# Kernel tuning notes

Measured on AMD Instinct MI355X. Metric: run time of the kernel, lower is better.

The kernel has to match this reference:

```python
import jax, jax.numpy as jnp
import numpy as np

N = 500000     # total nodes across all sets
DIM = 128      # input feature dim
HID = 128      # hidden_dim (output of key_net/val_net)
KDIM = 128     # key_storage.encoder.input_dim
MID = 128      # build_mlp mid width (midmult=1.0 -> (in+out)/2)
NB = 4096      # n_batches

def mish(x):
    return x * jnp.tanh(jax.nn.softplus(x))

def layernorm(x, g, b):
    mu = jnp.mean(x, axis=-1, keepdims=True)
    var = jnp.var(x, axis=-1, keepdims=True)
    return (x - mu) * jax.lax.rsqrt(var + 1e-5) * g + b

def mlp2(x, W1, b1, g, bn, W2, b2):
    # build_mlp(nlayers=2, layernorm=True, nonlinearity=Mish)
    h = layernorm(x @ W1 + b1, g, bn)
    return mish(h) @ W2 + b2

def seg_softmax(x, batch, n):
    # scatter_softmax over the node axis within each segment, per feature
    m = jax.ops.segment_max(x, batch, num_segments=n)
    e = jnp.exp(x - m[batch])
    d = jax.ops.segment_sum(e, batch, num_segments=n)
    return e / d[batch]

def _init(key, fan_in, shape):
    return jax.random.normal(key, shape, dtype=jnp.float32) / np.sqrt(fan_in)

def setup_inputs():
    key = jax.random.key(0)
    ks = jax.random.split(key, 12)
    return {
        "x": jax.random.normal(ks[0], (N, DIM), dtype=jnp.float32),
        "batch": jnp.sort(jax.random.randint(ks[1], (N,), 0, NB)),
        "n_batches": NB,
        # mapping: Linear(dim -> KDIM)
        "W_map": _init(ks[2], DIM, (DIM, KDIM)), "b_map": jnp.zeros(KDIM, jnp.float32),
        # key_net: KDIM -> MID -> HID
        "kW1": _init(ks[3], KDIM, (KDIM, MID)), "kb1": jnp.zeros(MID, jnp.float32),
        "kg": jnp.ones(MID, jnp.float32), "kbn": jnp.zeros(MID, jnp.float32),
        "kW2": _init(ks[4], MID, (MID, HID)), "kb2": jnp.zeros(HID, jnp.float32),
        # val_net: DIM -> MID -> HID
        "vW1": _init(ks[5], DIM, (DIM, MID)), "vb1": jnp.zeros(MID, jnp.float32),
        "vg": jnp.ones(MID, jnp.float32), "vbn": jnp.zeros(MID, jnp.float32),
        "vW2": _init(ks[6], MID, (MID, HID)), "vb2": jnp.zeros(HID, jnp.float32),
        # inner key_storage encoder params (same structure, on keys)
        "iW_map": _init(ks[7], KDIM, (KDIM, KDIM)), "ib_map": jnp.zeros(KDIM, jnp.float32),
        "ikW1": _init(ks[8], KDIM, (KDIM, MID)), "ikb1": jnp.zeros(MID, jnp.float32),
        "ikg": jnp.ones(MID, jnp.float32), "ikbn": jnp.zeros(MID, jnp.float32),
        "ikW2": _init(ks[9], MID, (MID, HID)), "ikb2": jnp.zeros(HID, jnp.float32),
        "ivW1": _init(ks[10], KDIM, (KDIM, MID)), "ivb1": jnp.zeros(MID, jnp.float32),
        "ivg": jnp.ones(MID, jnp.float32), "ivbn": jnp.zeros(MID, jnp.float32),
        "ivW2": _init(ks[11], MID, (MID, HID)), "ivb2": jnp.zeros(HID, jnp.float32),
    }

def reference(x, batch, n_batches, W_map, b_map, kW1, kb1, kg, kbn, kW2, kb2,
              vW1, vb1, vg, vbn, vW2, vb2, iW_map, ib_map,
              ikW1, ikb1, ikg, ikbn, ikW2, ikb2, ivW1, ivb1, ivg, ivbn, ivW2, ivb2):
    # key0 = mapping(x); keys = scatter_softmax(key0, batch)
    key0 = x @ W_map + b_map                      # [N, KDIM]
    keys = seg_softmax(key0, batch, n_batches)    # [N, KDIM]
    # y = val_net(x) * key_net(keys); z = scatter_sum(y, batch)
    y = mlp2(x, vW1, vb1, vg, vbn, vW2, vb2) * mlp2(keys, kW1, kb1, kg, kbn, kW2, kb2)
    z = jax.ops.segment_sum(y, batch, num_segments=n_batches)   # [NB, HID]
    # keyenc = key_storage.encoder(keys, batch): same encoder math applied to keys
    key0b = keys @ iW_map + ib_map
    keys2 = seg_softmax(key0b, batch, n_batches)
    y2 = mlp2(keys, ivW1, ivb1, ivg, ivbn, ivW2, ivb2) * mlp2(keys2, ikW1, ikb1, ikg, ikbn, ikW2, ikb2)
    keyenc = jax.ops.segment_sum(y2, batch, num_segments=n_batches)  # [NB, HID]
    return (z, keyenc)
```

## Files before the change

### kernel.cpp

```cpp
#include <hip/hip_runtime.h>

typedef _Float16 f16;
typedef _Float16 f16x4 __attribute__((ext_vector_type(4)));
typedef _Float16 f16x8 __attribute__((ext_vector_type(8)));
typedef float f32x4 __attribute__((ext_vector_type(4)));

#define NBATCH 4096
#define RMAX 200

__device__ __forceinline__ f32x4 mfma16(f16x8 a, f16x8 b, f32x4 c) {
  return __builtin_amdgcn_mfma_f32_16x16x32_f16(a, b, c, 0, 0, 0);
}

__device__ __forceinline__ int swz(int r, int c) { return r * 128 + (c ^ ((r & 7) << 3)); }

__global__ void seg_bounds(const int* __restrict__ batch, int N, int NB, int* __restrict__ seg) {
  int s = blockIdx.x * blockDim.x + threadIdx.x;
  if (s > NB) return;
  int lo = 0, hi = N;
  while (lo < hi) { int mid = (lo + hi) >> 1; if (batch[mid] < s) lo = mid + 1; else hi = mid; }
  seg[s] = lo;
}

__global__ void pack_weights(const float* w0, const float* w1, const float* w2, const float* w3,
                             const float* w4, const float* w5, const float* w6, const float* w7,
                             const float* w8, const float* w9, f16* __restrict__ Wp) {
  int idx = blockIdx.x * blockDim.x + threadIdx.x;
  if (idx >= 10 * 16384) return;
  int w = idx >> 14, p = idx & 16383;
  int j = p & 7, lane = (p >> 3) & 63, nt = (p >> 9) & 7, kk = p >> 12;
  int k = kk * 32 + (lane >> 4) * 8 + j;
  int n = nt * 16 + (lane & 15);
  const float* W;
  switch (w) {
    case 0: W = w0; break; case 1: W = w1; break; case 2: W = w2; break;
    case 3: W = w3; break; case 4: W = w4; break; case 5: W = w5; break;
    case 6: W = w6; break; case 7: W = w7; break; case 8: W = w8; break;
    default: W = w9; break;
  }
  Wp[idx] = (f16)W[k * 128 + n];
}

__device__ __forceinline__ void gemm_bias_phase(const f16* S, f16* D, const f16* __restrict__ Wg,
    const float* __restrict__ bias, int rows, int mq, int nq, int lane, int quad, int li) {
  int ntl = (rows + 15) >> 4;
  const f16* wb0 = Wg + (size_t)(((nq * 2 + 0) * 64 + lane) * 8);
  const f16* wb1 = Wg + (size_t)(((nq * 2 + 1) * 64 + lane) * 8);
  float bc0 = bias[(nq * 2 + 0) * 16 + li];
  float bc1 = bias[(nq * 2 + 1) * 16 + li];
  for (int t = mq; t < ntl; t += 4) {
    int m0 = t * 16;
    f32x4 acc0 = {0.f, 0.f, 0.f, 0.f}, acc1 = {0.f, 0.f, 0.f, 0.f};
    int rl = m0 + li;
    bool ok = rl < rows;
#pragma unroll
    for (int kk = 0; kk < 4; ++kk) {
      f16x8 aF = {};
      if (ok) aF = *(const f16x8*)(S + swz(rl, kk * 32 + quad * 8));
      f16x8 b0 = *(const f16x8*)(wb0 + kk * 4096);
      f16x8 b1 = *(const f16x8*)(wb1 + kk * 4096);
      acc0 = mfma16(aF, b0, acc0);
      acc1 = mfma16(aF, b1, acc1);
    }
#pragma unroll
    for (int r = 0; r < 4; ++r) {
      int row = m0 + quad * 4 + r;
      if (row < rows) {
        D[swz(row, (nq * 2) * 16 + li)] = (f16)(acc0[r] + bc0);
        D[swz(row, (nq * 2 + 1) * 16 + li)] = (f16)(acc1[r] + bc1);
      }
    }
  }
}

__device__ __forceinline__ void ln_mish_pass(f16* D, const float* __restrict__ g,
                                             const float* __restrict__ bn, int rows, int tid) {
  int part = tid & 7;
  int cbase = part * 16;
  for (int r = tid >> 3; r < rows; r += 128) {
    f16x8 v0 = *(const f16x8*)(D + swz(r, cbase));
    f16x8 v1 = *(const f16x8*)(D + swz(r, cbase + 8));
    float f[16];
#pragma unroll
    for (int e = 0; e < 8; ++e) { f[e] = (float)v0[e]; f[8 + e] = (float)v1[e]; }
    float s1 = 0.f, s2 = 0.f;
#pragma unroll
    for (int e = 0; e < 16; ++e) { s1 += f[e]; s2 = fmaf(f[e], f[e], s2); }
    s1 += __shfl_xor(s1, 1, 64); s2 += __shfl_xor(s2, 1, 64);
    s1 += __shfl_xor(s1, 2, 64); s2 += __shfl_xor(s2, 2, 64);
    s1 += __shfl_xor(s1, 4, 64); s2 += __shfl_xor(s2, 4, 64);
    float mean = s1 * (1.f / 128.f);
    float var = s2 * (1.f / 128.f) - mean * mean;
    float rstd = rsqrtf(var + 1e-5f);
    float mr = -mean * rstd;
    f16x8 o0, o1;
#pragma unroll
    for (int e = 0; e < 16; ++e) {
      float gv = g[cbase + e];
      float bv = bn[cbase + e];
      float u = fmaf(fmaf(f[e], rstd, mr), gv, bv);
      float t = __expf(u);
      float w = t * t + 2.f * t;
      float res = (u > 20.f) ? u : u * (w / (w + 2.f));
      if (e < 8) o0[e] = (f16)res; else o1[e - 8] = (f16)res;
    }
    *(f16x8*)(D + swz(r, cbase)) = o0;
    *(f16x8*)(D + swz(r, cbase + 8)) = o1;
  }
}

__device__ __forceinline__ void softmax_phase(f16* P, int rows, int tid,
                                              float* __restrict__ pm, float* __restrict__ mbuf) {
  int cg = tid & 15, st = tid >> 4;
  int c8 = cg * 8;
  int wv = tid >> 6;
  f16x8 NEGV;
#pragma unroll
  for (int e = 0; e < 8; ++e) NEGV[e] = (f16)(-65504.f);
  int r0 = st, r1 = st + 64, r2 = st + 128, r3 = st + 192;
  f16x8 v0 = (r0 < rows) ? *(const f16x8*)(P + swz(r0, c8)) : NEGV;
  f16x8 v1 = (r1 < rows) ? *(const f16x8*)(P + swz(r1, c8)) : NEGV;
  f16x8 v2 = (r2 < rows) ? *(const f16x8*)(P + swz(r2, c8)) : NEGV;
  f16x8 v3 = (r3 < rows) ? *(const f16x8*)(P + swz(r3, c8)) : NEGV;
  float m8[8];
#pragma unroll
  for (int e = 0; e < 8; ++e) {
    float a = (float)v0[e], b = (float)v1[e], c = (float)v2[e], d = (float)v3[e];
    m8[e] = fmaxf(fmaxf(a, b), fmaxf(c, d));
    m8[e] = fmaxf(m8[e], __shfl_xor(m8[e], 16, 64));
    m8[e] = fmaxf(m8[e], __shfl_xor(m8[e], 32, 64));
  }
  if ((tid & 63) < 16) {
    float4 pa = {m8[0], m8[1], m8[2], m8[3]}, pb = {m8[4], m8[5], m8[6], m8[7]};
    *(float4*)(pm + wv * 128 + c8) = pa;
    *(float4*)(pm + wv * 128 + c8 + 4) = pb;
  }
  __syncthreads();
  if (tid < 128) {
    float M = pm[tid];
#pragma unroll
    for (int w = 1; w < 16; ++w) M = fmaxf(M, pm[w * 128 + tid]);
    mbuf[tid] = M;
  }
  __syncthreads();
  float M8[8];
  {
    float4 a = *(const float4*)(mbuf + c8);
    float4 b = *(const float4*)(mbuf + c8 + 4);
    M8[0] = a.x; M8[1] = a.y; M8[2] = a.z; M8[3] = a.w;
    M8[4] = b.x; M8[5] = b.y; M8[6] = b.z; M8[7] = b.w;
  }
  float d8[8];
#pragma unroll
  for (int e = 0; e < 8; ++e) {
    float s = __expf((float)v0[e] - M8[e]) + __expf((float)v1[e] - M8[e]) +
              __expf((float)v2[e] - M8[e]) + __expf((float)v3[e] - M8[e]);
    s += __shfl_xor(s, 16, 64);
    s += __shfl_xor(s, 32, 64);
    d8[e] = s;
  }
  __syncthreads();
  if ((tid & 63) < 16) {
    float4 pa = {d8[0], d8[1], d8[2], d8[3]}, pb = {d8[4], d8[5], d8[6], d8[7]};
    *(float4*)(pm + wv * 128 + c8) = pa;
    *(float4*)(pm + wv * 128 + c8 + 4) = pb;
  }
  __syncthreads();
  if (tid < 128) {
    float Dv = 0.f;
#pragma unroll
    for (int w = 0; w < 16; ++w) Dv += pm[w * 128 + tid];
    mbuf[tid] = (Dv > 0.f) ? 1.f / Dv : 0.f;
  }
  __syncthreads();
  float I8[8];
  {
    float4 a = *(const float4*)(mbuf + c8);
    float4 b = *(const float4*)(mbuf + c8 + 4);
    I8[0] = a.x; I8[1] = a.y; I8[2] = a.z; I8[3] = a.w;
    I8[4] = b.x; I8[5] = b.y; I8[6] = b.z; I8[7] = b.w;
  }
  if (r0 < rows) {
    f16x8 o;
#pragma unroll
    for (int e = 0; e < 8; ++e) o[e] = (f16)(__expf((float)v0[e] - M8[e]) * I8[e]);
    *(f16x8*)(P + swz(r0, c8)) = o;
  }
  if (r1 < rows) {
    f16x8 o;
#pragma unroll
    for (int e = 0; e < 8; ++e) o[e] = (f16)(__expf((float)v1[e] - M8[e]) * I8[e]);
    *(f16x8*)(P + swz(r1, c8)) = o;
  }
  if (r2 < rows) {
    f16x8 o;
#pragma unroll
    for (int e = 0; e < 8; ++e) o[e] = (f16)(__expf((float)v2[e] - M8[e]) * I8[e]);
    *(f16x8*)(P + swz(r2, c8)) = o;
  }
  if (r3 < rows) {
    f16x8 o;
#pragma unroll
    for (int e = 0; e < 8; ++e) o[e] = (f16)(__expf((float)v3[e] - M8[e]) * I8[e]);
    *(f16x8*)(P + swz(r3, c8)) = o;
  }
}

__device__ __forceinline__ void pairsum_phase(const f16* S1, const f16* __restrict__ W1,
    const float* __restrict__ b1, const f16* S2, const f16* __restrict__ W2,
    const float* __restrict__ b2, float* __restrict__ outp, int s, int rows,
    int mq, int nq, int lane, int quad, int li, float* red, int tid) {
  const f16* w10 = W1 + (size_t)(((nq * 2 + 0) * 64 + lane) * 8);
  const f16* w11 = W1 + (size_t)(((nq * 2 + 1) * 64 + lane) * 8);
  const f16* w20 = W2 + (size_t)(((nq * 2 + 0) * 64 + lane) * 8);
  const f16* w21 = W2 + (size_t)(((nq * 2 + 1) * 64 + lane) * 8);
  float b1c0 = b1[(nq * 2 + 0) * 16 + li], b1c1 = b1[(nq * 2 + 1) * 16 + li];
  float b2c0 = b2[(nq * 2 + 0) * 16 + li], b2c1 = b2[(nq * 2 + 1) * 16 + li];
  float zs0 = 0.f, zs1 = 0.f;
  int ntl = (rows + 15) >> 4;
  for (int t = mq; t < ntl; t += 4) {
    int m0 = t * 16;
    f32x4 a10 = {0.f,0.f,0.f,0.f}, a11 = {0.f,0.f,0.f,0.f};
    f32x4 a20 = {0.f,0.f,0.f,0.f}, a21 = {0.f,0.f,0.f,0.f};
    int rl = m0 + li;
    bool ok = rl < rows;
#pragma unroll
    for (int kk = 0; kk < 4; ++kk) {
      f16x8 aF1 = {}, aF2 = {};
      if (ok) {
        aF1 = *(const f16x8*)(S1 + swz(rl, kk * 32 + quad * 8));
        aF2 = *(const f16x8*)(S2 + swz(rl, kk * 32 + quad * 8));
      }
      a10 = mfma16(aF1, *(const f16x8*)(w10 + kk * 4096), a10);
      a11 = mfma16(aF1, *(const f16x8*)(w11 + kk * 4096), a11);
      a20 = mfma16(aF2, *(const f16x8*)(w20 + kk * 4096), a20);
      a21 = mfma16(aF2, *(const f16x8*)(w21 + kk * 4096), a21);
    }
    float cs0 = 0.f, cs1 = 0.f;
#pragma unroll
    for (int r = 0; r < 4; ++r) {
      int row = m0 + quad * 4 + r;
      if (row < rows) {
        cs0 += (a10[r] + b1c0) * (a20[r] + b2c0);
        cs1 += (a11[r] + b1c1) * (a21[r] + b2c1);
      }
    }
    cs0 += __shfl_xor(cs0, 16, 64); cs0 += __shfl_xor(cs0, 32, 64);
    cs1 += __shfl_xor(cs1, 16, 64); cs1 += __shfl_xor(cs1, 32, 64);
    zs0 += cs0; zs1 += cs1;
  }
  if (quad == 0) {
    red[mq * 128 + nq * 32 + li] = zs0;
    red[mq * 128 + nq * 32 + 16 + li] = zs1;
  }
  __syncthreads();
  if (tid < 128) {
    float ssum = red[tid] + red[128 + tid] + red[256 + tid] + red[384 + tid];
    outp[(size_t)s * 128 + tid] = ssum;
  }
  __syncthreads();
}

__global__ __launch_bounds__(1024)
__attribute__((amdgpu_waves_per_eu(4, 4)))
void encoder_mega(
    const float* __restrict__ x, const int* __restrict__ seg, const f16* __restrict__ Wp,
    const float* b_map, const float* kb1, const float* kg, const float* kbn, const float* kb2,
    const float* vb1, const float* vg, const float* vbn, const float* vb2,
    const float* ib_map, const float* ikb1, const float* ikg, const float* ikbn,
    const float* ikb2, const float* ivb1, const float* ivg, const float* ivbn,
    const float* ivb2, float* __restrict__ Z, float* __restrict__ KE) {
  __shared__ f16 L0[RMAX * 128];
  __shared__ f16 L1[RMAX * 128];
  __shared__ f16 L2[RMAX * 128];
  __shared__ float pm[16 * 128];
  __shared__ float mbuf[128];
  int s = blockIdx.x;
  int a = seg[s], e = seg[s + 1];
  int rows = e - a;
  int tid = threadIdx.x;
  if (rows <= 0) {
    if (tid < 128) {
      Z[(size_t)s * 128 + tid] = 0.f;
      KE[(size_t)s * 128 + tid] = 0.f;
    }
    return;
  }
  if (rows > RMAX) rows = RMAX;
  int lane = tid & 63, wave = tid >> 6, quad = lane >> 4, li = lane & 15;
  int mq = wave & 3, nq = wave >> 2;

  const float* xa = x + (size_t)a * 128;
  for (int i = tid * 8; i < rows * 128; i += 8192) {
    float4 u0 = *(const float4*)(xa + i);
    float4 u1 = *(const float4*)(xa + i + 4);
    f16x8 h;
    h[0] = (f16)u0.x; h[1] = (f16)u0.y; h[2] = (f16)u0.z; h[3] = (f16)u0.w;
    h[4] = (f16)u1.x; h[5] = (f16)u1.y; h[6] = (f16)u1.z; h[7] = (f16)u1.w;
    *(f16x8*)(L0 + swz(i >> 7, i & 127)) = h;
  }
  __syncthreads();
  gemm_bias_phase(L0, L1, Wp + 0 * 16384, b_map, rows, mq, nq, lane, quad, li);
  __syncthreads();
  softmax_phase(L1, rows, tid, pm, mbuf);
  gemm_bias_phase(L0, L2, Wp + 3 * 16384, vb1, rows, mq, nq, lane, quad, li);
  __syncthreads();
  ln_mish_pass(L2, vg, vbn, rows, tid);
  __syncthreads();
  gemm_bias_phase(L1, L0, Wp + 1 * 16384, kb1, rows, mq, nq, lane, quad, li);
  __syncthreads();
  ln_mish_pass(L0, kg, kbn, rows, tid);
  __syncthreads();
  pairsum_phase(L2, Wp + 4 * 16384, vb2, L0, Wp + 2 * 16384, kb2, Z, s, rows,
                mq, nq, lane, quad, li, pm, tid);
  gemm_bias_phase(L1, L2, Wp + 5 * 16384, ib_map, rows, mq, nq, lane, quad, li);
  __syncthreads();
  softmax_phase(L2, rows, tid, pm, mbuf);
  gemm_bias_phase(L1, L0, Wp + 8 * 16384, ivb1, rows, mq, nq, lane, quad, li);
  __syncthreads();
  ln_mish_pass(L0, ivg, ivbn, rows, tid);
  __syncthreads();
  gemm_bias_phase(L2, L1, Wp + 6 * 16384, ikb1, rows, mq, nq, lane, quad, li);
  __syncthreads();
  ln_mish_pass(L1, ikg, ikbn, rows, tid);
  __syncthreads();
  pairsum_phase(L0, Wp + 9 * 16384, ivb2, L1, Wp + 7 * 16384, ikb2, KE, s, rows,
                mq, nq, lane, quad, li, pm, tid);
}

extern "C" void kernel_launch(void* const* d_in, const int* in_sizes, int n_in,
                              void* d_out, int out_size, void* d_ws, size_t ws_size,
                              hipStream_t stream) {
  const float* x = (const float*)d_in[0];
  const int* batch = (const int*)d_in[1];
  const int N = in_sizes[1];
  const float* W_map = (const float*)d_in[3];  const float* b_map = (const float*)d_in[4];
  const float* kW1 = (const float*)d_in[5];    const float* kb1 = (const float*)d_in[6];
  const float* kg = (const float*)d_in[7];     const float* kbn = (const float*)d_in[8];
  const float* kW2 = (const float*)d_in[9];    const float* kb2 = (const float*)d_in[10];
  const float* vW1 = (const float*)d_in[11];   const float* vb1 = (const float*)d_in[12];
  const float* vg = (const float*)d_in[13];    const float* vbn = (const float*)d_in[14];
  const float* vW2 = (const float*)d_in[15];   const float* vb2 = (const float*)d_in[16];
  const float* iW_map = (const float*)d_in[17];const float* ib_map = (const float*)d_in[18];
  const float* ikW1 = (const float*)d_in[19];  const float* ikb1 = (const float*)d_in[20];
  const float* ikg = (const float*)d_in[21];   const float* ikbn = (const float*)d_in[22];
  const float* ikW2 = (const float*)d_in[23];  const float* ikb2 = (const float*)d_in[24];
  const float* ivW1 = (const float*)d_in[25];  const float* ivb1 = (const float*)d_in[26];
  const float* ivg = (const float*)d_in[27];   const float* ivbn = (const float*)d_in[28];
  const float* ivW2 = (const float*)d_in[29];  const float* ivb2 = (const float*)d_in[30];

  char* ws = (char*)d_ws;
  int* seg = (int*)ws;
  f16* Wp = (f16*)(ws + 32768);

  float* Z = (float*)d_out;
  float* KE = Z + (out_size / 2);

  seg_bounds<<<(NBATCH + 1 + 255) / 256, 256, 0, stream>>>(batch, N, NBATCH, seg);
  pack_weights<<<(10 * 16384) / 256, 256, 0, stream>>>(
      W_map, kW1, kW2, vW1, vW2, iW_map, ikW1, ikW2, ivW1, ivW2, Wp);

  encoder_mega<<<NBATCH, 1024, 0, stream>>>(
      x, seg, Wp, b_map, kb1, kg, kbn, kb2, vb1, vg, vbn, vb2,
      ib_map, ikb1, ikg, ikbn, ikb2, ivb1, ivg, ivbn, ivb2, Z, KE);
}
```

Measured before the change: 1.098 ms.

## Fuse sibling GEMMs sharing an input and cache softmax exponentials

Two pairs of GEMMs that read the same LDS input (mapping plus val first layer, and inner mapping plus inner val first layer) are merged into one dual-GEMM pass. Each A fragment is then loaded once and feeds four MFMAs, and one barrier per pair is dropped. The segmented softmax now stores the exponentials back into its registers as f16 and reuses them for the normalised output instead of calling exp a second time. In exchange, the fused loop uses more registers (four accumulators), there is a slight precision change from rounding the exponentials to f16 before normalising, and the phase order around the second softmax and LN is adjusted with an extra trailing barrier.

```diff
diff --git a/kernel.cpp b/kernel.cpp
--- a/kernel.cpp
+++ b/kernel.cpp
@@ -57,10 +57,8 @@
     for (int kk = 0; kk < 4; ++kk) {
       f16x8 aF = {};
       if (ok) aF = *(const f16x8*)(S + swz(rl, kk * 32 + quad * 8));
-      f16x8 b0 = *(const f16x8*)(wb0 + kk * 4096);
-      f16x8 b1 = *(const f16x8*)(wb1 + kk * 4096);
-      acc0 = mfma16(aF, b0, acc0);
-      acc1 = mfma16(aF, b1, acc1);
+      acc0 = mfma16(aF, *(const f16x8*)(wb0 + kk * 4096), acc0);
+      acc1 = mfma16(aF, *(const f16x8*)(wb1 + kk * 4096), acc1);
     }
 #pragma unroll
     for (int r = 0; r < 4; ++r) {
@@ -68,6 +66,45 @@
       if (row < rows) {
         D[swz(row, (nq * 2) * 16 + li)] = (f16)(acc0[r] + bc0);
         D[swz(row, (nq * 2 + 1) * 16 + li)] = (f16)(acc1[r] + bc1);
+      }
+    }
+  }
+}
+
+__device__ __forceinline__ void dual_gemm_phase(const f16* S, f16* D1, f16* D2,
+    const f16* __restrict__ W1, const float* __restrict__ b1,
+    const f16* __restrict__ W2, const float* __restrict__ b2,
+    int rows, int mq, int nq, int lane, int quad, int li) {
+  int ntl = (rows + 15) >> 4;
+  const f16* w10 = W1 + (size_t)(((nq * 2 + 0) * 64 + lane) * 8);
+  const f16* w11 = W1 + (size_t)(((nq * 2 + 1) * 64 + lane) * 8);
+  const f16* w20 = W2 + (size_t)(((nq * 2 + 0) * 64 + lane) * 8);
+  const f16* w21 = W2 + (size_t)(((nq * 2 + 1) * 64 + lane) * 8);
+  float b1c0 = b1[(nq * 2 + 0) * 16 + li], b1c1 = b1[(nq * 2 + 1) * 16 + li];
+  float b2c0 = b2[(nq * 2 + 0) * 16 + li], b2c1 = b2[(nq * 2 + 1) * 16 + li];
+  for (int t = mq; t < ntl; t += 4) {
+    int m0 = t * 16;
+    f32x4 a10 = {0.f,0.f,0.f,0.f}, a11 = {0.f,0.f,0.f,0.f};
+    f32x4 a20 = {0.f,0.f,0.f,0.f}, a21 = {0.f,0.f,0.f,0.f};
+    int rl = m0 + li;
+    bool ok = rl < rows;
+#pragma unroll
+    for (int kk = 0; kk < 4; ++kk) {
+      f16x8 aF = {};
+      if (ok) aF = *(const f16x8*)(S + swz(rl, kk * 32 + quad * 8));
+      a10 = mfma16(aF, *(const f16x8*)(w10 + kk * 4096), a10);
+      a11 = mfma16(aF, *(const f16x8*)(w11 + kk * 4096), a11);
+      a20 = mfma16(aF, *(const f16x8*)(w20 + kk * 4096), a20);
+      a21 = mfma16(aF, *(const f16x8*)(w21 + kk * 4096), a21);
+    }
+#pragma unroll
+    for (int r = 0; r < 4; ++r) {
+      int row = m0 + quad * 4 + r;
+      if (row < rows) {
+        D1[swz(row, (nq * 2) * 16 + li)] = (f16)(a10[r] + b1c0);
+        D1[swz(row, (nq * 2 + 1) * 16 + li)] = (f16)(a11[r] + b1c1);
+        D2[swz(row, (nq * 2) * 16 + li)] = (f16)(a20[r] + b2c0);
+        D2[swz(row, (nq * 2 + 1) * 16 + li)] = (f16)(a21[r] + b2c1);
       }
     }
   }
@@ -143,21 +180,23 @@
     mbuf[tid] = M;
   }
   __syncthreads();
-  float M8[8];
+  float d8[8];
   {
     float4 a = *(const float4*)(mbuf + c8);
     float4 b = *(const float4*)(mbuf + c8 + 4);
-    M8[0] = a.x; M8[1] = a.y; M8[2] = a.z; M8[3] = a.w;
-    M8[4] = b.x; M8[5] = b.y; M8[6] = b.z; M8[7] = b.w;
-  }
-  float d8[8];
-#pragma unroll
-  for (int e = 0; e < 8; ++e) {
-    float s = __expf((float)v0[e] - M8[e]) + __expf((float)v1[e] - M8[e]) +
-              __expf((float)v2[e] - M8[e]) + __expf((float)v3[e] - M8[e]);
-    s += __shfl_xor(s, 16, 64);
-    s += __shfl_xor(s, 32, 64);
-    d8[e] = s;
+    float M8[8] = {a.x, a.y, a.z, a.w, b.x, b.y, b.z, b.w};
+#pragma unroll
+    for (int e = 0; e < 8; ++e) {
+      float e0 = __expf((float)v0[e] - M8[e]);
+      float e1 = __expf((float)v1[e] - M8[e]);
+      float e2 = __expf((float)v2[e] - M8[e]);
+      float e3 = __expf((float)v3[e] - M8[e]);
+      v0[e] = (f16)e0; v1[e] = (f16)e1; v2[e] = (f16)e2; v3[e] = (f16)e3;
+      float s = (e0 + e1) + (e2 + e3);
+      s += __shfl_xor(s, 16, 64);
+      s += __shfl_xor(s, 32, 64);
+      d8[e] = s;
+    }
   }
   __syncthreads();
   if ((tid & 63) < 16) {
@@ -183,27 +222,28 @@
   if (r0 < rows) {
     f16x8 o;
 #pragma unroll
-    for (int e = 0; e < 8; ++e) o[e] = (f16)(__expf((float)v0[e] - M8[e]) * I8[e]);
+    for (int e = 0; e < 8; ++e) o[e] = (f16)((float)v0[e] * I8[e]);
     *(f16x8*)(P + swz(r0, c8)) = o;
   }
   if (r1 < rows) {
     f16x8 o;
 #pragma unroll
-    for (int e = 0; e < 8; ++e) o[e] = (f16)(__expf((float)v1[e] - M8[e]) * I8[e]);
+    for (int e = 0; e < 8; ++e) o[e] = (f16)((float)v1[e] * I8[e]);
     *(f16x8*)(P + swz(r1, c8)) = o;
   }
   if (r2 < rows) {
     f16x8 o;
 #pragma unroll
-    for (int e = 0; e < 8; ++e) o[e] = (f16)(__expf((float)v2[e] - M8[e]) * I8[e]);
+    for (int e = 0; e < 8; ++e) o[e] = (f16)((float)v2[e] * I8[e]);
     *(f16x8*)(P + swz(r2, c8)) = o;
   }
   if (r3 < rows) {
     f16x8 o;
 #pragma unroll
-    for (int e = 0; e < 8; ++e) o[e] = (f16)(__expf((float)v3[e] - M8[e]) * I8[e]);
+    for (int e = 0; e < 8; ++e) o[e] = (f16)((float)v3[e] * I8[e]);
     *(f16x8*)(P + swz(r3, c8)) = o;
   }
+  __syncthreads();
 }
 
 __device__ __forceinline__ void pairsum_phase(const f16* S1, const f16* __restrict__ W1,
@@ -261,8 +301,7 @@
   __syncthreads();
 }
 
-__global__ __launch_bounds__(1024)
-__attribute__((amdgpu_waves_per_eu(4, 4)))
+__global__ __attribute__((amdgpu_flat_work_group_size(1024, 1024), amdgpu_waves_per_eu(4, 4)))
 void encoder_mega(
     const float* __restrict__ x, const int* __restrict__ seg, const f16* __restrict__ Wp,
     const float* b_map, const float* kb1, const float* kg, const float* kbn, const float* kb2,
@@ -300,11 +339,10 @@
     *(f16x8*)(L0 + swz(i >> 7, i & 127)) = h;
   }
   __syncthreads();
-  gemm_bias_phase(L0, L1, Wp + 0 * 16384, b_map, rows, mq, nq, lane, quad, li);
+  dual_gemm_phase(L0, L1, L2, Wp + 0 * 16384, b_map, Wp + 3 * 16384, vb1,
+                  rows, mq, nq, lane, quad, li);
   __syncthreads();
   softmax_phase(L1, rows, tid, pm, mbuf);
-  gemm_bias_phase(L0, L2, Wp + 3 * 16384, vb1, rows, mq, nq, lane, quad, li);
-  __syncthreads();
   ln_mish_pass(L2, vg, vbn, rows, tid);
   __syncthreads();
   gemm_bias_phase(L1, L0, Wp + 1 * 16384, kb1, rows, mq, nq, lane, quad, li);
@@ -313,13 +351,11 @@
   __syncthreads();
   pairsum_phase(L2, Wp + 4 * 16384, vb2, L0, Wp + 2 * 16384, kb2, Z, s, rows,
                 mq, nq, lane, quad, li, pm, tid);
-  gemm_bias_phase(L1, L2, Wp + 5 * 16384, ib_map, rows, mq, nq, lane, quad, li);
-  __syncthreads();
+  dual_gemm_phase(L1, L2, L0, Wp + 5 * 16384, ib_map, Wp + 8 * 16384, ivb1,
+                  rows, mq, nq, lane, quad, li);
+  __syncthreads();
+  ln_mish_pass(L0, ivg, ivbn, rows, tid);
   softmax_phase(L2, rows, tid, pm, mbuf);
-  gemm_bias_phase(L1, L0, Wp + 8 * 16384, ivb1, rows, mq, nq, lane, quad, li);
-  __syncthreads();
-  ln_mish_pass(L0, ivg, ivbn, rows, tid);
-  __syncthreads();
   gemm_bias_phase(L2, L1, Wp + 6 * 16384, ikb1, rows, mq, nq, lane, quad, li);
   __syncthreads();
   ln_mish_pass(L1, ikg, ikbn, rows, tid);
```

Result: slower. 1.140 ms (+3.9%).
